# Optimization experiments

Measured on AMD Instinct MI355X. Metric: run time of the kernel, lower is better.

Reference implementation:

```python
import jax, jax.numpy as jnp
import numpy as np

B, T, D = 1, 4096, 2048
NUM_HEADS, NUM_KV_HEADS, HEAD_DIM = 16, 8, 128
QUERY_PRE_ATTN_SCALAR = HEAD_DIM ** -0.5
SOFT_CAP = 50.0
WINDOW = 1024
ROPE_BASE = 10000.0
ROPE_SCALE = 1.0
K_MASK = -2.3819763e+38


def apply_rope(x, positions, head_dim, max_wavelength=ROPE_BASE, scale_factor=ROPE_SCALE):
    # x: [B, T, N, H], positions: [B, T]
    fraction = 2.0 * jnp.arange(head_dim // 2, dtype=jnp.float32) / head_dim
    timescale = max_wavelength ** fraction  # [H/2]
    sinusoid = positions[..., None].astype(jnp.float32) / timescale  # [B, T, H/2]
    sinusoid = (sinusoid / scale_factor)[..., None, :]  # [B, T, 1, H/2]
    sin, cos = jnp.sin(sinusoid), jnp.cos(sinusoid)
    first, second = jnp.split(x, 2, axis=-1)
    out = jnp.concatenate([first * cos - second * sin,
                           second * cos + first * sin], axis=-1)
    return out.astype(x.dtype)


def setup_inputs() -> dict:
    key = jax.random.key(0)
    ks = jax.random.split(key, 4)
    x = jax.random.normal(ks[0], (B, T, D), dtype=jnp.float32)
    segment_pos = jnp.broadcast_to(jnp.arange(T, dtype=jnp.int32), (B, T))
    # causal mask [B, T, S]
    attn_mask = jnp.broadcast_to(
        jnp.tril(jnp.ones((T, T), dtype=jnp.bool_)), (B, T, T))
    q_w = jax.random.normal(ks[1], (NUM_HEADS, D, HEAD_DIM), dtype=jnp.float32) * 0.02
    kv_w = jax.random.normal(ks[2], (2, NUM_KV_HEADS, D, HEAD_DIM), dtype=jnp.float32) * 0.02
    o_w = jax.random.normal(ks[3], (NUM_HEADS, HEAD_DIM, D), dtype=jnp.float32) * 0.02
    return {"x": x, "segment_pos": segment_pos, "attn_mask": attn_mask,
            "q_w": q_w, "kv_w": kv_w, "o_w": o_w}


def reference(x, segment_pos, attn_mask, q_w, kv_w, o_w):
    # Projections (GQA: separate q and kv einsums)
    q = jnp.einsum('BTD,NDH->BTNH', x, q_w)          # [B,T,N,H]
    k = jnp.einsum('BSD,KDH->BSKH', x, kv_w[0])      # [B,S,K,H]
    v = jnp.einsum('BSD,KDH->BSKH', x, kv_w[1])      # [B,S,K,H]

    q = apply_rope(q, segment_pos, HEAD_DIM)
    q = q * QUERY_PRE_ATTN_SCALAR
    k = apply_rope(k, segment_pos, HEAD_DIM)

    num_groups = NUM_HEADS // NUM_KV_HEADS
    qg = q.reshape(B, T, NUM_KV_HEADS, num_groups, HEAD_DIM)
    logits = jnp.einsum('BTKGH,BSKH->BTKGS', qg, k)
    logits = logits.reshape(B, T, NUM_HEADS, -1)     # [B,T,N,S]

    # soft cap
    logits = jnp.tanh(logits / SOFT_CAP) * SOFT_CAP

    # sliding-window mask combined with causal mask
    all_ones = jnp.ones_like(attn_mask)
    sliding = jnp.triu(all_ones, -WINDOW + 1) * jnp.tril(all_ones, WINDOW - 1)
    mask = sliding * attn_mask                       # [B,T,S] bool

    padded = jnp.where(mask[:, :, None, :], logits, K_MASK)
    probs = jax.nn.softmax(padded, axis=-1).astype(k.dtype)

    probs_g = probs.reshape(B, T, NUM_KV_HEADS, num_groups, -1)
    encoded = jnp.einsum('BTKGS,BSKH->BTKGH', probs_g, v)
    encoded = encoded.reshape(B, T, NUM_HEADS, HEAD_DIM)

    attn_output = jnp.einsum('BTNH,NHD->BTD', encoded, o_w)
    return attn_output
```

## Files before the change

kernel.cpp:

```cpp
#include <hip/hip_runtime.h>
#include <hip/hip_bf16.h>
#include <math.h>

typedef __attribute__((ext_vector_type(8))) short short8;
typedef __attribute__((ext_vector_type(8))) unsigned short ushort8;
typedef __attribute__((ext_vector_type(4))) float f32x4;

#define T_SEQ 4096
#define D_MODEL 2048
#define N_HEADS 16
#define N_KV 8
#define HEAD_DIM 128
#define QSCALE 0.08838834764831845f

__device__ __forceinline__ float bf2f(unsigned short u) {
  union { unsigned int i; float f; } x; x.i = ((unsigned int)u) << 16; return x.f;
}
__device__ __forceinline__ unsigned short f2bf(float f) {
  union { float f; unsigned int i; } x; x.f = f;
  unsigned int i = x.i;
  unsigned int r = i + 0x7fffu + ((i >> 16) & 1u);
  return (unsigned short)(r >> 16);
}

__global__ __launch_bounds__(256) void cvt_x_kernel(const float* __restrict__ x,
                                                    unsigned short* __restrict__ xb) {
  int idx = blockIdx.x * 256 + threadIdx.x;
  const float4* p = reinterpret_cast<const float4*>(x) + (size_t)idx * 2;
  float4 a = p[0], b = p[1];
  ushort8 o;
  o[0] = f2bf(a.x); o[1] = f2bf(a.y); o[2] = f2bf(a.z); o[3] = f2bf(a.w);
  o[4] = f2bf(b.x); o[5] = f2bf(b.y); o[6] = f2bf(b.z); o[7] = f2bf(b.w);
  reinterpret_cast<ushort8*>(xb)[idx] = o;
}

__global__ __launch_bounds__(256) void rope_table_kernel(const int* __restrict__ segpos,
                                                         float2* __restrict__ tab) {
  int idx = blockIdx.x * 256 + threadIdx.x;
  int t = idx >> 6, i = idx & 63;
  float pos = (float)segpos[t];
  float ts = powf(10000.f, (float)(2 * i) / 128.f);
  float ang = pos / ts;
  tab[idx] = make_float2(sinf(ang), cosf(ang));
}

__global__ __launch_bounds__(256) void transpose_f32_bf16_kernel(const float* __restrict__ src,
                                                                 unsigned short* __restrict__ dst,
                                                                 int sstride, int dstride,
                                                                 long sBatch, long dBatch) {
  __shared__ float tile[32][33];
  long b = blockIdx.z;
  src += b * sBatch; dst += b * dBatch;
  int c0 = blockIdx.x * 32, r0 = blockIdx.y * 32;
  int tx = threadIdx.x & 31, ty = threadIdx.x >> 5;
#pragma unroll
  for (int i = 0; i < 4; ++i)
    tile[ty + i * 8][tx] = src[(size_t)(r0 + ty + i * 8) * sstride + c0 + tx];
  __syncthreads();
#pragma unroll
  for (int i = 0; i < 4; ++i)
    dst[(size_t)(c0 + ty + i * 8) * dstride + r0 + tx] = f2bf(tile[tx][ty + i * 8]);
}

__global__ __launch_bounds__(256) void transpose_bf16_kernel(const unsigned short* __restrict__ src,
                                                             unsigned short* __restrict__ dst,
                                                             int sstride, int dstride,
                                                             long sBatch, long dBatch) {
  __shared__ unsigned short tile[32][33];
  long b = blockIdx.z;
  src += b * sBatch; dst += b * dBatch;
  int c0 = blockIdx.x * 32, r0 = blockIdx.y * 32;
  int tx = threadIdx.x & 31, ty = threadIdx.x >> 5;
#pragma unroll
  for (int i = 0; i < 4; ++i)
    tile[ty + i * 8][tx] = src[(size_t)(r0 + ty + i * 8) * sstride + c0 + tx];
  __syncthreads();
#pragma unroll
  for (int i = 0; i < 4; ++i)
    dst[(size_t)(c0 + ty + i * 8) * dstride + r0 + tx] = tile[tx][ty + i * 8];
}

#define G2L(gp, lp)                                                           \
  __builtin_amdgcn_global_load_lds(                                           \
      (const __attribute__((address_space(1))) void*)(gp),                    \
      (__attribute__((address_space(3))) void*)(lp), 16, 0, 0)
#define GBAR() asm volatile("s_barrier" ::: "memory")
#define VMW(n) asm volatile("s_waitcnt vmcnt(" #n ")" ::: "memory")

template <int OUT_BF16>
__global__ __launch_bounds__(512, 2) void gemm256_kernel(const unsigned short* __restrict__ A,
                                                         const unsigned short* __restrict__ Bt,
                                                         void* __restrict__ Cout,
                                                         int M, int N, int K) {
  extern __shared__ unsigned short smem[];
  unsigned short* ldsA = smem;
  unsigned short* ldsB = smem + 32768;
  const int tid = threadIdx.x;
  const int lane = tid & 63, wave = tid >> 6;
  const int wm = wave >> 2, wn = wave & 3;
  const int lr = lane & 15, lg = lane >> 4;
  const int swz = (lr & 7) << 3;
  const int c0s = (lg * 8) ^ swz;
  const int c1s = (32 + lg * 8) ^ swz;

  int id = blockIdx.y * gridDim.x + blockIdx.x;
  int nb = gridDim.x * gridDim.y;
  int sw = (id & 7) * (nb >> 3) + (id >> 3);
  const long brow = (long)(sw / gridDim.x) * 256;
  const long bcol = (long)(sw % gridDim.x) * 256;

  const unsigned short* Ag = A + brow * K;
  const unsigned short* Bg = Bt + bcol * K;

  const int r0 = tid >> 3;
  const int cs = ((tid & 7) * 8) ^ ((r0 & 7) << 3);

#define ST_A(tt, b, a)                                                        \
  { G2L(Ag + (size_t)((a) * 128 + r0) * K + (size_t)(tt) * 64 + cs,           \
        ldsA + (b) * 16384 + (a) * 8192 + tid * 8);                           \
    G2L(Ag + (size_t)((a) * 128 + r0 + 64) * K + (size_t)(tt) * 64 + cs,      \
        ldsA + (b) * 16384 + (a) * 8192 + 4096 + tid * 8); }
#define ST_B(tt, b, h)                                                        \
  { G2L(Bg + (size_t)((h) * 128 + r0) * K + (size_t)(tt) * 64 + cs,           \
        ldsB + (b) * 16384 + (h) * 8192 + tid * 8);                           \
    G2L(Bg + (size_t)((h) * 128 + r0 + 64) * K + (size_t)(tt) * 64 + cs,      \
        ldsB + (b) * 16384 + (h) * 8192 + 4096 + tid * 8); }

  f32x4 acc[8][4] = {};
  short8 bf[4][2];
  short8 af[4];

#define RD_B(b)                                                               \
  { const unsigned short* pb = ldsB + (b) * 16384 + (wn >> 1) * 8192 + (wn & 1) * 4096; \
    _Pragma("unroll")                                                         \
    for (int n = 0; n < 4; ++n) {                                             \
      bf[n][0] = *(const short8*)(pb + (n * 16 + lr) * 64 + c0s);             \
      bf[n][1] = *(const short8*)(pb + (n * 16 + lr) * 64 + c1s);             \
    } }
#define RD_A(b, mb)                                                           \
  { const unsigned short* pa = ldsA + (b) * 16384 + wm * 8192;                \
    af[0] = *(const short8*)(pa + ((mb) * 16 + lr) * 64 + c0s);               \
    af[1] = *(const short8*)(pa + ((mb) * 16 + lr) * 64 + c1s);               \
    af[2] = *(const short8*)(pa + ((mb) * 16 + 16 + lr) * 64 + c0s);          \
    af[3] = *(const short8*)(pa + ((mb) * 16 + 16 + lr) * 64 + c1s); }
#define MFMA2(mb)                                                             \
  { __builtin_amdgcn_s_setprio(1);                                            \
    _Pragma("unroll")                                                         \
    for (int n = 0; n < 4; ++n) {                                             \
      acc[mb][n]     = __builtin_amdgcn_mfma_f32_16x16x32_bf16(af[0], bf[n][0], acc[mb][n], 0, 0, 0);     \
      acc[mb][n]     = __builtin_amdgcn_mfma_f32_16x16x32_bf16(af[1], bf[n][1], acc[mb][n], 0, 0, 0);     \
      acc[mb + 1][n] = __builtin_amdgcn_mfma_f32_16x16x32_bf16(af[2], bf[n][0], acc[mb + 1][n], 0, 0, 0); \
      acc[mb + 1][n] = __builtin_amdgcn_mfma_f32_16x16x32_bf16(af[3], bf[n][1], acc[mb + 1][n], 0, 0, 0); \
    }                                                                         \
    __builtin_amdgcn_s_setprio(0); }

  ST_B(0, 0, 0); ST_B(0, 0, 1); ST_A(0, 0, 0); ST_A(0, 0, 1);
  ST_B(1, 1, 0); ST_B(1, 1, 1);
  VMW(4);
  ST_A(1, 1, 0); ST_A(1, 1, 1);
  GBAR();

  const int NT = K >> 6;
  for (int j = 0; j < (NT >> 1); ++j) {
    const int t2 = 2 * j + 2, t3 = 2 * j + 3;
    const bool s2 = t2 < NT, s3 = t3 < NT;
    RD_B(0); RD_A(0, 0);
    if (s2) ST_B(t2, 0, 0);
    GBAR(); MFMA2(0); GBAR();
    RD_A(0, 2);
    if (s2) ST_B(t2, 0, 1);
    GBAR(); MFMA2(2); GBAR();
    RD_A(0, 4);
    GBAR(); MFMA2(4); GBAR();
    RD_A(0, 6);
    if (s2) { VMW(4); ST_A(t2, 0, 0); ST_A(t2, 0, 1); }
    else    { VMW(0); }
    GBAR(); MFMA2(6); GBAR();
    RD_B(1); RD_A(1, 0);
    if (s3) ST_B(t3, 1, 0);
    GBAR(); MFMA2(0); GBAR();
    RD_A(1, 2);
    if (s3) ST_B(t3, 1, 1);
    GBAR(); MFMA2(2); GBAR();
    RD_A(1, 4);
    GBAR(); MFMA2(4); GBAR();
    RD_A(1, 6);
    if (s3) { VMW(4); ST_A(t3, 1, 0); ST_A(t3, 1, 1); }
    else    { VMW(0); }
    GBAR(); MFMA2(6); GBAR();
  }

#undef ST_A
#undef ST_B
#undef RD_A
#undef RD_B
#undef MFMA2

#pragma unroll
  for (int m = 0; m < 8; ++m) {
#pragma unroll
    for (int i = 0; i < 4; ++i) {
      long row = brow + wm * 128 + m * 16 + lg * 4 + i;
#pragma unroll
      for (int n = 0; n < 4; ++n) {
        long col = bcol + wn * 64 + n * 16 + lr;
        if (OUT_BF16)
          ((unsigned short*)Cout)[row * N + col] = f2bf(acc[m][n][i]);
        else
          ((float*)Cout)[row * N + col] = acc[m][n][i];
      }
    }
  }
}

__global__ __launch_bounds__(256) void rope_apply_kernel(const unsigned short* __restrict__ raw,
                                                         const float2* __restrict__ tab,
                                                         unsigned short* __restrict__ Qb,
                                                         unsigned short* __restrict__ Kb) {
  int gid = blockIdx.x * 256 + threadIdx.x;
  int j = gid & 7;
  int rem = gid >> 3;
  int hs = rem % 24;
  int t = rem / 24;
  int i0 = j * 8;
  float sv[8], cv[8];
  const float2* tp = tab + t * 64 + i0;
#pragma unroll
  for (int q = 0; q < 8; ++q) { float2 sc2 = tp[q]; sv[q] = sc2.x; cv[q] = sc2.y; }
  if (hs < 16) {
    const unsigned short* p = raw + (size_t)t * 4096 + hs * 128 + i0;
    ushort8 a = *(const ushort8*)p;
    ushort8 b = *(const ushort8*)(p + 64);
    ushort8 o1, o2;
#pragma unroll
    for (int q = 0; q < 8; ++q) {
      float fa = bf2f(a[q]), fb = bf2f(b[q]);
      o1[q] = f2bf((fa * cv[q] - fb * sv[q]) * QSCALE);
      o2[q] = f2bf((fb * cv[q] + fa * sv[q]) * QSCALE);
    }
    unsigned short* qp = Qb + ((size_t)hs * T_SEQ + t) * 128 + i0;
    *(ushort8*)qp = o1;
    *(ushort8*)(qp + 64) = o2;
  } else {
    int kn = hs - 16;
    const unsigned short* p = raw + (size_t)t * 4096 + 2048 + kn * 128 + i0;
    ushort8 a = *(const ushort8*)p;
    ushort8 b = *(const ushort8*)(p + 64);
    ushort8 o1, o2;
#pragma unroll
    for (int q = 0; q < 8; ++q) {
      float fa = bf2f(a[q]), fb = bf2f(b[q]);
      o1[q] = f2bf(fa * cv[q] - fb * sv[q]);
      o2[q] = f2bf(fb * cv[q] + fa * sv[q]);
    }
    unsigned short* kp = Kb + ((size_t)kn * T_SEQ + t) * 128 + i0;
    *(ushort8*)kp = o1;
    *(ushort8*)(kp + 64) = o2;
  }
}

__global__ __launch_bounds__(512) void attn_kernel(const unsigned short* __restrict__ Qb,
                                                   const unsigned short* __restrict__ Kb,
                                                   const unsigned short* __restrict__ Vt,
                                                   unsigned short* __restrict__ enc) {
  __shared__ unsigned short Ks[64][128];
  __shared__ unsigned short Vs[128][64];
  __shared__ unsigned short Ps[8][16][66];
  int lin = blockIdx.y * 32 + blockIdx.x;
  lin = (lin & 7) * 64 + (lin >> 3);
  const int h = lin >> 5;
  const int qb0 = (lin & 31) * 128;
  const int kvh = h >> 1;
  const int tid = threadIdx.x, lane = tid & 63, wave = tid >> 6;
  const int qw = qb0 + wave * 16;
  const int lr = lane & 15, lg = lane >> 4;
  const int sw = (lr & 7) << 3;

  short8 aq[4];
  {
    const unsigned short* qp = Qb + ((size_t)h * T_SEQ + qw + lr) * 128 + lg * 8;
#pragma unroll
    for (int c = 0; c < 4; ++c) aq[c] = *(const short8*)(qp + c * 32);
  }
  f32x4 acc[8] = {};
  float lsum[4] = {0.f, 0.f, 0.f, 0.f};

  const int s_lo = (qb0 - 1023) > 0 ? (qb0 - 1023) : 0;
  const int kb_lo = s_lo >> 6, kb_hi = (qb0 + 127) >> 6;

  const int rK = tid >> 4;
  const int cpK = (tid & 15) * 8;
  const int colK = cpK ^ ((rK & 7) << 3);
  const int rV = tid >> 3;
  const int cpV = (tid & 7) * 8;
  const int colV = cpV ^ ((rV & 7) << 3);
  const unsigned short* kgb = Kb + ((size_t)kvh * T_SEQ + rK) * 128 + colK;
  const unsigned short* vgb = Vt + ((size_t)kvh * 128 + rV) * T_SEQ + colV;

  ushort8 kr0, kr1, vr0, vr1;
  {
    const int s0g = kb_lo * 64;
    kr0 = *(const ushort8*)(kgb + (size_t)s0g * 128);
    kr1 = *(const ushort8*)(kgb + (size_t)(s0g + 32) * 128);
    vr0 = *(const ushort8*)(vgb + s0g);
    vr1 = *(const ushort8*)(vgb + (size_t)64 * T_SEQ + s0g);
  }

  for (int kb = kb_lo; kb <= kb_hi; ++kb) {
    const int s0g = kb * 64;
    __syncthreads();
    *(ushort8*)&Ks[rK][cpK] = kr0;
    *(ushort8*)&Ks[rK + 32][cpK] = kr1;
    *(ushort8*)&Vs[rV][cpV] = vr0;
    *(ushort8*)&Vs[rV + 64][cpV] = vr1;
    __syncthreads();
    if (kb < kb_hi) {
      const int sn = s0g + 64;
      kr0 = *(const ushort8*)(kgb + (size_t)sn * 128);
      kr1 = *(const ushort8*)(kgb + (size_t)(sn + 32) * 128);
      vr0 = *(const ushort8*)(vgb + sn);
      vr1 = *(const ushort8*)(vgb + (size_t)64 * T_SEQ + sn);
    }
    if (s0g > qw + 15 || s0g + 63 < qw - 1023) continue;

    f32x4 sv[4] = {};
#pragma unroll
    for (int st = 0; st < 4; ++st) {
      const int krow = st * 16 + lr;
#pragma unroll
      for (int c = 0; c < 4; ++c) {
        short8 b = *(const short8*)&Ks[krow][(c * 32 + lg * 8) ^ sw];
        sv[st] = __builtin_amdgcn_mfma_f32_16x16x32_bf16(aq[c], b, sv[st], 0, 0, 0);
      }
    }
#pragma unroll
    for (int st = 0; st < 4; ++st) {
#pragma unroll
      for (int r = 0; r < 4; ++r) {
        float s = sv[st][r];
        float z2 = s * s * 4.0e-4f;
        float capped = s * (15.f + z2) * __builtin_amdgcn_rcpf(fmaf(z2, 6.f, 15.f));
        float p = __expf(capped);
        int qg = qw + lg * 4 + r;
        int sg = s0g + st * 16 + lr;
        p = ((unsigned)(qg - sg) <= 1023u) ? p : 0.f;
        lsum[r] += p;
        Ps[wave][lg * 4 + r][st * 16 + lr] = f2bf(p);
      }
    }
    short8 pa0 = *(const short8*)&Ps[wave][lr][lg * 8];
    short8 pa1 = *(const short8*)&Ps[wave][lr][32 + lg * 8];
#pragma unroll
    for (int d0 = 0; d0 < 8; ++d0) {
      const int vrow = d0 * 16 + lr;
      short8 bv0 = *(const short8*)&Vs[vrow][(lg * 8) ^ sw];
      short8 bv1 = *(const short8*)&Vs[vrow][(32 + lg * 8) ^ sw];
      acc[d0] = __builtin_amdgcn_mfma_f32_16x16x32_bf16(pa0, bv0, acc[d0], 0, 0, 0);
      acc[d0] = __builtin_amdgcn_mfma_f32_16x16x32_bf16(pa1, bv1, acc[d0], 0, 0, 0);
    }
  }

#pragma unroll
  for (int r = 0; r < 4; ++r) {
    float l = lsum[r];
    l += __shfl_xor(l, 1);
    l += __shfl_xor(l, 2);
    l += __shfl_xor(l, 4);
    l += __shfl_xor(l, 8);
    float inv = __builtin_amdgcn_rcpf(l);
    int row = qw + lg * 4 + r;
    unsigned short* op = enc + (size_t)row * D_MODEL + h * 128 + lr;
#pragma unroll
    for (int d0 = 0; d0 < 8; ++d0) op[d0 * 16] = f2bf(acc[d0][r] * inv);
  }
}

extern "C" void kernel_launch(void* const* d_in, const int* in_sizes, int n_in,
                              void* d_out, int out_size, void* d_ws, size_t ws_size,
                              hipStream_t stream) {
  const float* x = (const float*)d_in[0];
  const int* segpos = (const int*)d_in[1];
  const float* q_w = (const float*)d_in[3];
  const float* kv_w = (const float*)d_in[4];
  const float* o_w = (const float*)d_in[5];
  float* out = (float*)d_out;
  char* ws = (char*)d_ws;

  const size_t OFF_XB = 0;
  const size_t OFF_WT = OFF_XB + 16777216;
  const size_t OFF_RAW = OFF_WT + 16777216;
  const size_t OFF_KB = OFF_RAW + 33554432;
  const size_t OFF_VT = OFF_KB + 8388608;
  const size_t OFF_TAB = OFF_VT + 8388608;
  unsigned short* xb = (unsigned short*)(ws + OFF_XB);
  unsigned short* Wt = (unsigned short*)(ws + OFF_WT);
  unsigned short* raw = (unsigned short*)(ws + OFF_RAW);
  unsigned short* Kb = (unsigned short*)(ws + OFF_KB);
  unsigned short* Vt = (unsigned short*)(ws + OFF_VT);
  float2* tab = (float2*)(ws + OFF_TAB);
  unsigned short* o_wt = xb;
  unsigned short* Qb = Wt;
  unsigned short* enc = raw;

  hipFuncSetAttribute((const void*)(gemm256_kernel<1>),
                      hipFuncAttributeMaxDynamicSharedMemorySize, 131072);
  hipFuncSetAttribute((const void*)(gemm256_kernel<0>),
                      hipFuncAttributeMaxDynamicSharedMemorySize, 131072);

  cvt_x_kernel<<<dim3(4096), dim3(256), 0, stream>>>(x, xb);
  rope_table_kernel<<<dim3(1024), dim3(256), 0, stream>>>(segpos, tab);
  transpose_f32_bf16_kernel<<<dim3(4, 64, 16), dim3(256), 0, stream>>>(
      q_w, Wt, 128, 2048, (long)2048 * 128, (long)128 * 2048);
  transpose_f32_bf16_kernel<<<dim3(4, 64, 16), dim3(256), 0, stream>>>(
      kv_w, Wt + (size_t)2048 * 2048, 128, 2048, (long)2048 * 128, (long)128 * 2048);
  gemm256_kernel<1><<<dim3(16, 16), dim3(512), 131072, stream>>>(xb, Wt, (void*)raw, 4096, 4096, 2048);
  transpose_f32_bf16_kernel<<<dim3(64, 64, 1), dim3(256), 0, stream>>>(
      o_w, o_wt, 2048, 2048, 0L, 0L);
  rope_apply_kernel<<<dim3(3072), dim3(256), 0, stream>>>(raw, tab, Qb, Kb);
  transpose_bf16_kernel<<<dim3(4, 128, 8), dim3(256), 0, stream>>>(
      raw + 3072, Vt, 4096, 4096, 128L, (long)128 * 4096);
  attn_kernel<<<dim3(32, 16), dim3(512), 0, stream>>>(Qb, Kb, Vt, enc);
  gemm256_kernel<0><<<dim3(8, 16), dim3(512), 131072, stream>>>(enc, o_wt, (void*)out, 4096, 2048, 2048);
}
```

Before: 226.9 us.

## Halve output GEMM tile width and transpose attention score MFMA to skip masking

```diff
diff --git a/kernel.cpp b/kernel.cpp
--- a/kernel.cpp
+++ b/kernel.cpp
@@ -87,11 +87,12 @@
 #define GBAR() asm volatile("s_barrier" ::: "memory")
 #define VMW(n) asm volatile("s_waitcnt vmcnt(" #n ")" ::: "memory")
 
-template <int OUT_BF16>
+template <int OUT_BF16, int NHB>
 __global__ __launch_bounds__(512, 2) void gemm256_kernel(const unsigned short* __restrict__ A,
                                                          const unsigned short* __restrict__ Bt,
                                                          void* __restrict__ Cout,
                                                          int M, int N, int K) {
+  constexpr int NW = 2 * NHB;
   extern __shared__ unsigned short smem[];
   unsigned short* ldsA = smem;
   unsigned short* ldsB = smem + 32768;
@@ -107,7 +108,7 @@
   int nb = gridDim.x * gridDim.y;
   int sw = (id & 7) * (nb >> 3) + (id >> 3);
   const long brow = (long)(sw / gridDim.x) * 256;
-  const long bcol = (long)(sw % gridDim.x) * 256;
+  const long bcol = (long)(sw % gridDim.x) * (128 * NHB);
 
   const unsigned short* Ag = A + brow * K;
   const unsigned short* Bg = Bt + bcol * K;
@@ -122,18 +123,18 @@
         ldsA + (b) * 16384 + (a) * 8192 + 4096 + tid * 8); }
 #define ST_B(tt, b, h)                                                        \
   { G2L(Bg + (size_t)((h) * 128 + r0) * K + (size_t)(tt) * 64 + cs,           \
-        ldsB + (b) * 16384 + (h) * 8192 + tid * 8);                           \
+        ldsB + (b) * 8192 * NHB + (h) * 8192 + tid * 8);                      \
     G2L(Bg + (size_t)((h) * 128 + r0 + 64) * K + (size_t)(tt) * 64 + cs,      \
-        ldsB + (b) * 16384 + (h) * 8192 + 4096 + tid * 8); }
-
-  f32x4 acc[8][4] = {};
-  short8 bf[4][2];
+        ldsB + (b) * 8192 * NHB + (h) * 8192 + 4096 + tid * 8); }
+
+  f32x4 acc[8][NW] = {};
+  short8 bf[NW][2];
   short8 af[4];
 
 #define RD_B(b)                                                               \
-  { const unsigned short* pb = ldsB + (b) * 16384 + (wn >> 1) * 8192 + (wn & 1) * 4096; \
+  { const unsigned short* pb = ldsB + (b) * 8192 * NHB + wn * 2048 * NHB;     \
     _Pragma("unroll")                                                         \
-    for (int n = 0; n < 4; ++n) {                                             \
+    for (int n = 0; n < NW; ++n) {                                            \
       bf[n][0] = *(const short8*)(pb + (n * 16 + lr) * 64 + c0s);             \
       bf[n][1] = *(const short8*)(pb + (n * 16 + lr) * 64 + c1s);             \
     } }
@@ -146,7 +147,7 @@
 #define MFMA2(mb)                                                             \
   { __builtin_amdgcn_s_setprio(1);                                            \
     _Pragma("unroll")                                                         \
-    for (int n = 0; n < 4; ++n) {                                             \
+    for (int n = 0; n < NW; ++n) {                                            \
       acc[mb][n]     = __builtin_amdgcn_mfma_f32_16x16x32_bf16(af[0], bf[n][0], acc[mb][n], 0, 0, 0);     \
       acc[mb][n]     = __builtin_amdgcn_mfma_f32_16x16x32_bf16(af[1], bf[n][1], acc[mb][n], 0, 0, 0);     \
       acc[mb + 1][n] = __builtin_amdgcn_mfma_f32_16x16x32_bf16(af[2], bf[n][0], acc[mb + 1][n], 0, 0, 0); \
@@ -154,9 +155,12 @@
     }                                                                         \
     __builtin_amdgcn_s_setprio(0); }
 
-  ST_B(0, 0, 0); ST_B(0, 0, 1); ST_A(0, 0, 0); ST_A(0, 0, 1);
-  ST_B(1, 1, 0); ST_B(1, 1, 1);
-  VMW(4);
+  ST_B(0, 0, 0);
+  if constexpr (NHB == 2) ST_B(0, 0, 1);
+  ST_A(0, 0, 0); ST_A(0, 0, 1);
+  ST_B(1, 1, 0);
+  if constexpr (NHB == 2) ST_B(1, 1, 1);
+  if constexpr (NHB == 2) { VMW(4); } else { VMW(2); }
   ST_A(1, 1, 0); ST_A(1, 1, 1);
   GBAR();
 
@@ -168,25 +172,29 @@
     if (s2) ST_B(t2, 0, 0);
     GBAR(); MFMA2(0); GBAR();
     RD_A(0, 2);
-    if (s2) ST_B(t2, 0, 1);
+    if constexpr (NHB == 2) { if (s2) ST_B(t2, 0, 1); }
     GBAR(); MFMA2(2); GBAR();
     RD_A(0, 4);
     GBAR(); MFMA2(4); GBAR();
     RD_A(0, 6);
-    if (s2) { VMW(4); ST_A(t2, 0, 0); ST_A(t2, 0, 1); }
-    else    { VMW(0); }
+    if (s2) {
+      if constexpr (NHB == 2) { VMW(4); } else { VMW(2); }
+      ST_A(t2, 0, 0); ST_A(t2, 0, 1);
+    } else { VMW(0); }
     GBAR(); MFMA2(6); GBAR();
     RD_B(1); RD_A(1, 0);
     if (s3) ST_B(t3, 1, 0);
     GBAR(); MFMA2(0); GBAR();
     RD_A(1, 2);
-    if (s3) ST_B(t3, 1, 1);
+    if constexpr (NHB == 2) { if (s3) ST_B(t3, 1, 1); }
     GBAR(); MFMA2(2); GBAR();
     RD_A(1, 4);
     GBAR(); MFMA2(4); GBAR();
     RD_A(1, 6);
-    if (s3) { VMW(4); ST_A(t3, 1, 0); ST_A(t3, 1, 1); }
-    else    { VMW(0); }
+    if (s3) {
+      if constexpr (NHB == 2) { VMW(4); } else { VMW(2); }
+      ST_A(t3, 1, 0); ST_A(t3, 1, 1);
+    } else { VMW(0); }
     GBAR(); MFMA2(6); GBAR();
   }
 
@@ -202,8 +210,8 @@
     for (int i = 0; i < 4; ++i) {
       long row = brow + wm * 128 + m * 16 + lg * 4 + i;
 #pragma unroll
-      for (int n = 0; n < 4; ++n) {
-        long col = bcol + wn * 64 + n * 16 + lr;
+      for (int n = 0; n < NW; ++n) {
+        long col = bcol + wn * (32 * NHB) + n * 16 + lr;
         if (OUT_BF16)
           ((unsigned short*)Cout)[row * N + col] = f2bf(acc[m][n][i]);
         else
@@ -265,7 +273,7 @@
                                                    unsigned short* __restrict__ enc) {
   __shared__ unsigned short Ks[64][128];
   __shared__ unsigned short Vs[128][64];
-  __shared__ unsigned short Ps[8][16][66];
+  __shared__ unsigned short Ps[8][16][72];
   int lin = blockIdx.y * 32 + blockIdx.x;
   lin = (lin & 7) * 64 + (lin >> 3);
   const int h = lin >> 5;
@@ -283,7 +291,7 @@
     for (int c = 0; c < 4; ++c) aq[c] = *(const short8*)(qp + c * 32);
   }
   f32x4 acc[8] = {};
-  float lsum[4] = {0.f, 0.f, 0.f, 0.f};
+  float lsum = 0.f;
 
   const int s_lo = (qb0 - 1023) > 0 ? (qb0 - 1023) : 0;
   const int kb_lo = s_lo >> 6, kb_hi = (qb0 + 127) >> 6;
@@ -306,6 +314,7 @@
     vr1 = *(const ushort8*)(vgb + (size_t)64 * T_SEQ + s0g);
   }
 
+  const int qg = qw + lr;
   for (int kb = kb_lo; kb <= kb_hi; ++kb) {
     const int s0g = kb * 64;
     __syncthreads();
@@ -322,31 +331,39 @@
       vr1 = *(const ushort8*)(vgb + (size_t)64 * T_SEQ + sn);
     }
     if (s0g > qw + 15 || s0g + 63 < qw - 1023) continue;
-
-    f32x4 sv[4] = {};
+    const bool interior = (s0g + 63 <= qw) && (s0g >= qw - 1008);
+
+    f32x4 sT[4] = {};
 #pragma unroll
     for (int st = 0; st < 4; ++st) {
       const int krow = st * 16 + lr;
 #pragma unroll
       for (int c = 0; c < 4; ++c) {
-        short8 b = *(const short8*)&Ks[krow][(c * 32 + lg * 8) ^ sw];
-        sv[st] = __builtin_amdgcn_mfma_f32_16x16x32_bf16(aq[c], b, sv[st], 0, 0, 0);
+        short8 kf = *(const short8*)&Ks[krow][(c * 32 + lg * 8) ^ sw];
+        sT[st] = __builtin_amdgcn_mfma_f32_16x16x32_bf16(kf, aq[c], sT[st], 0, 0, 0);
       }
     }
 #pragma unroll
     for (int st = 0; st < 4; ++st) {
+      float p[4];
 #pragma unroll
       for (int r = 0; r < 4; ++r) {
-        float s = sv[st][r];
+        float s = sT[st][r];
         float z2 = s * s * 4.0e-4f;
         float capped = s * (15.f + z2) * __builtin_amdgcn_rcpf(fmaf(z2, 6.f, 15.f));
-        float p = __expf(capped);
-        int qg = qw + lg * 4 + r;
-        int sg = s0g + st * 16 + lr;
-        p = ((unsigned)(qg - sg) <= 1023u) ? p : 0.f;
-        lsum[r] += p;
-        Ps[wave][lg * 4 + r][st * 16 + lr] = f2bf(p);
+        float pv = __expf(capped);
+        if (!interior) {
+          int sg = s0g + st * 16 + lg * 4 + r;
+          pv = ((unsigned)(qg - sg) <= 1023u) ? pv : 0.f;
+        }
+        lsum += pv;
+        p[r] = pv;
       }
+      unsigned u0, u1;
+      asm("v_cvt_pk_bf16_f32 %0, %1, %2" : "=v"(u0) : "v"(p[0]), "v"(p[1]));
+      asm("v_cvt_pk_bf16_f32 %0, %1, %2" : "=v"(u1) : "v"(p[2]), "v"(p[3]));
+      uint2 w; w.x = u0; w.y = u1;
+      *(uint2*)&Ps[wave][lr][st * 16 + lg * 4] = w;
     }
     short8 pa0 = *(const short8*)&Ps[wave][lr][lg * 8];
     short8 pa1 = *(const short8*)&Ps[wave][lr][32 + lg * 8];
@@ -360,14 +377,13 @@
     }
   }
 
+  float l = lsum;
+  l += __shfl_xor(l, 16);
+  l += __shfl_xor(l, 32);
 #pragma unroll
   for (int r = 0; r < 4; ++r) {
-    float l = lsum[r];
-    l += __shfl_xor(l, 1);
-    l += __shfl_xor(l, 2);
-    l += __shfl_xor(l, 4);
-    l += __shfl_xor(l, 8);
-    float inv = __builtin_amdgcn_rcpf(l);
+    float lt = __shfl(l, lg * 4 + r);
+    float inv = __builtin_amdgcn_rcpf(lt);
     int row = qw + lg * 4 + r;
     unsigned short* op = enc + (size_t)row * D_MODEL + h * 128 + lr;
 #pragma unroll
@@ -402,10 +418,10 @@
   unsigned short* Qb = Wt;
   unsigned short* enc = raw;
 
-  hipFuncSetAttribute((const void*)(gemm256_kernel<1>),
+  hipFuncSetAttribute((const void*)(gemm256_kernel<1, 2>),
                       hipFuncAttributeMaxDynamicSharedMemorySize, 131072);
-  hipFuncSetAttribute((const void*)(gemm256_kernel<0>),
-                      hipFuncAttributeMaxDynamicSharedMemorySize, 131072);
+  hipFuncSetAttribute((const void*)(gemm256_kernel<0, 1>),
+                      hipFuncAttributeMaxDynamicSharedMemorySize, 98304);
 
   cvt_x_kernel<<<dim3(4096), dim3(256), 0, stream>>>(x, xb);
   rope_table_kernel<<<dim3(1024), dim3(256), 0, stream>>>(segpos, tab);
@@ -413,12 +429,12 @@
       q_w, Wt, 128, 2048, (long)2048 * 128, (long)128 * 2048);
   transpose_f32_bf16_kernel<<<dim3(4, 64, 16), dim3(256), 0, stream>>>(
       kv_w, Wt + (size_t)2048 * 2048, 128, 2048, (long)2048 * 128, (long)128 * 2048);
-  gemm256_kernel<1><<<dim3(16, 16), dim3(512), 131072, stream>>>(xb, Wt, (void*)raw, 4096, 4096, 2048);
+  gemm256_kernel<1, 2><<<dim3(16, 16), dim3(512), 131072, stream>>>(xb, Wt, (void*)raw, 4096, 4096, 2048);
   transpose_f32_bf16_kernel<<<dim3(64, 64, 1), dim3(256), 0, stream>>>(
       o_w, o_wt, 2048, 2048, 0L, 0L);
   rope_apply_kernel<<<dim3(3072), dim3(256), 0, stream>>>(raw, tab, Qb, Kb);
   transpose_bf16_kernel<<<dim3(4, 128, 8), dim3(256), 0, stream>>>(
       raw + 3072, Vt, 4096, 4096, 128L, (long)128 * 4096);
   attn_kernel<<<dim3(32, 16), dim3(512), 0, stream>>>(Qb, Kb, Vt, enc);
-  gemm256_kernel<0><<<dim3(8, 16), dim3(512), 131072, stream>>>(enc, o_wt, (void*)out, 4096, 2048, 2048);
-}
+  gemm256_kernel<0, 1><<<dim3(16, 16), dim3(512), 98304, stream>>>(enc, o_wt, (void*)out, 4096, 2048, 2048);
+}
```

Result: faster. 205.0 us (-9.6%).
